# Kernel optimization log

Measured on AMD Instinct MI355X. Metric: run time of the kernel, lower is better.

The kernel has to match this reference:

```python
import jax, jax.numpy as jnp
import numpy as np

B, T, H = 8192, 24, 1024


def setup_inputs() -> dict:
    key = jax.random.key(0)
    ks = jax.random.split(key, 16)
    n = lambda k, shp, s=1.0: (jax.random.normal(k, shp, dtype=jnp.float32) * s)
    return {
        "x": n(ks[0], (B, T, 1)),
        "h1_0": n(ks[1], (B, H), 0.02),
        "c1_0": n(ks[2], (B, H), 0.02),
        "h2_0": n(ks[3], (B, H), 0.02),
        "c2_0": n(ks[4], (B, H), 0.02),
        "W_ih1": n(ks[5], (4 * H, 1), 0.05),
        "W_hh1": n(ks[6], (4 * H, H), 0.02),
        "b_ih1": n(ks[7], (4 * H,), 0.02),
        "b_hh1": n(ks[8], (4 * H,), 0.02),
        "W_ih2": n(ks[9], (4 * H, H), 0.02),
        "W_hh2": n(ks[10], (4 * H, H), 0.02),
        "b_ih2": n(ks[11], (4 * H,), 0.02),
        "b_hh2": n(ks[12], (4 * H,), 0.02),
        "W_out": n(ks[13], (2, H), 0.02),
        "b_out": jnp.array([0.2, -0.2], dtype=jnp.float32),
    }


def _lstm_cell(x_t, h, c, W_ih, W_hh, b_ih, b_hh):
    # PyTorch LSTMCell: gates ordered (i, f, g, o)
    gates = x_t @ W_ih.T + b_ih + h @ W_hh.T + b_hh  # [B, 4H]
    i, f, g, o = jnp.split(gates, 4, axis=-1)
    c_new = jax.nn.sigmoid(f) * c + jax.nn.sigmoid(i) * jnp.tanh(g)
    h_new = jax.nn.sigmoid(o) * jnp.tanh(c_new)
    return h_new, c_new


def reference(x, h1_0, c1_0, h2_0, c2_0,
              W_ih1, W_hh1, b_ih1, b_hh1,
              W_ih2, W_hh2, b_ih2, b_hh2,
              W_out, b_out):
    xs = jnp.transpose(x, (1, 0, 2))  # [T, B, 1]

    def step(carry, x_t):
        h1, c1, h2, c2 = carry
        h1, c1 = _lstm_cell(x_t, h1, c1, W_ih1, W_hh1, b_ih1, b_hh1)
        h2, c2 = _lstm_cell(h1, h2, c2, W_ih2, W_hh2, b_ih2, b_hh2)
        return (h1, c1, h2, c2), None

    (h1, c1, h2, c2), _ = jax.lax.scan(step, (h1_0, c1_0, h2_0, c2_0), xs)
    return h2 @ W_out.T + b_out  # [B, 2]
```

## Files before the change

kernel.cpp:

```cpp
#include <hip/hip_runtime.h>
#include <hip/hip_bf16.h>
#include <stdint.h>

#define B_SZ 8192
#define T_SZ 24
#define H_SZ 1024
#define G4   4096

typedef __attribute__((ext_vector_type(8))) short bf16x8;
typedef __attribute__((ext_vector_type(4))) float f32x4;

__device__ __forceinline__ int perm_old(int p) {
    int gate = (p >> 4) & 3;
    int unit = ((p >> 6) << 4) | (p & 15);
    return gate * 1024 + unit;
}

__global__ void k_prep_w1(const float* __restrict__ Whh1, __hip_bfloat16* __restrict__ dst) {
    int i = blockIdx.x * blockDim.x + threadIdx.x;
    int p = i >> 10, k = i & 1023;
    dst[i] = __float2bfloat16(Whh1[(size_t)perm_old(p) * 1024 + k]);
}

__global__ void k_prep_w2(const float* __restrict__ Wih2, const float* __restrict__ Whh2,
                          __hip_bfloat16* __restrict__ dst) {
    int i = blockIdx.x * blockDim.x + threadIdx.x;
    int p = i >> 11, k = i & 2047;
    int old = perm_old(p);
    float v = (k < 1024) ? Wih2[(size_t)old * 1024 + k] : Whh2[(size_t)old * 1024 + (k - 1024)];
    dst[i] = __float2bfloat16(v);
}

__global__ void k_prep_vec(const float* __restrict__ bih1, const float* __restrict__ bhh1,
                           const float* __restrict__ bih2, const float* __restrict__ bhh2,
                           const float* __restrict__ Wih1,
                           float* __restrict__ b1p, float* __restrict__ b2p,
                           float* __restrict__ w1p) {
    int p = blockIdx.x * blockDim.x + threadIdx.x;
    if (p >= G4) return;
    int old = perm_old(p);
    b1p[p] = bih1[old] + bhh1[old];
    b2p[p] = bih2[old] + bhh2[old];
    w1p[p] = Wih1[old];
}

__global__ void k_xT(const float* __restrict__ x, float* __restrict__ xT) {
    int i = blockIdx.x * blockDim.x + threadIdx.x;
    if (i >= B_SZ * T_SZ) return;
    int b = i / T_SZ, t = i % T_SZ;
    xT[t * B_SZ + b] = x[i];
}

__global__ void k_init_state(const float* __restrict__ h1_0, const float* __restrict__ c1_0,
                             const float* __restrict__ h2_0, const float* __restrict__ c2_0,
                             __hip_bfloat16* __restrict__ A2_0, __hip_bfloat16* __restrict__ A2_1,
                             float* __restrict__ c1, float* __restrict__ c2) {
    int i = blockIdx.x * blockDim.x + threadIdx.x;
    if (i >= B_SZ * H_SZ) return;
    int b = i >> 10, j = i & 1023;
    A2_1[(size_t)b * 2048 + j]        = __float2bfloat16(h1_0[i]);
    A2_0[(size_t)b * 2048 + 1024 + j] = __float2bfloat16(h2_0[i]);
    c1[i] = c1_0[i];
    c2[i] = c2_0[i];
}

#define BM 256
#define BN 256
#define BK 64

template<int LAYER>
__global__ __launch_bounds__(512, 2)
void k_gemm_cell(const __hip_bfloat16* __restrict__ A, int lda,
                 const __hip_bfloat16* __restrict__ Bw, int ldb, int K,
                 const float* __restrict__ biasp, const float* __restrict__ wih1p,
                 const float* __restrict__ xT, int t,
                 float* __restrict__ c, __hip_bfloat16* __restrict__ hout) {
    __shared__ short As[2][BM][BK];
    __shared__ short Bs[2][BN][BK];
    const int tid  = threadIdx.x;
    const int lane = tid & 63;
    const int wid  = tid >> 6;

    const int bid = blockIdx.x;
    const int xcd = bid & 7;
    const int i   = bid >> 3;
    const int ml  = (i & 7) | ((i >> 5) << 3);
    const int nl  = (i >> 3) & 3;
    const int m0  = ((xcd & 1) * 16 + ml) * BM;
    const int n0  = ((xcd >> 1) * 4 + nl) * BN;

    const int wm = wid >> 2;
    const int wn = wid & 3;
    const int fr = lane & 15;
    const int kg = lane >> 4;

    const __hip_bfloat16* Abase = A  + (size_t)m0 * lda;
    const __hip_bfloat16* Bbase = Bw + (size_t)n0 * ldb;

    f32x4 acc[8][4];
#pragma unroll
    for (int ii = 0; ii < 8; ++ii)
#pragma unroll
        for (int j = 0; j < 4; ++j) acc[ii][j] = (f32x4)0.f;

    auto stage8A = [&](int buf, int lr0, int kcol) {
        int lr = lr0 + (lane >> 3);
        int cr = lane & 7;
        int scol = ((cr ^ (lr & 7)) << 3);
        const __hip_bfloat16* gp = Abase + (size_t)lr * lda + kcol + scol;
        __builtin_amdgcn_global_load_lds(
            (const __attribute__((address_space(1))) void*)gp,
            (__attribute__((address_space(3))) void*)(&As[buf][lr0][0]), 16, 0, 0);
    };
    auto stage8B = [&](int buf, int lr0, int kcol) {
        int lr = lr0 + (lane >> 3);
        int cr = lane & 7;
        int scol = ((cr ^ (lr & 7)) << 3);
        const __hip_bfloat16* gp = Bbase + (size_t)lr * ldb + kcol + scol;
        __builtin_amdgcn_global_load_lds(
            (const __attribute__((address_space(1))) void*)gp,
            (__attribute__((address_space(3))) void*)(&Bs[buf][lr0][0]), 16, 0, 0);
    };
    auto stage_u1 = [&](int kt, int buf) {
#pragma unroll
        for (int j = 0; j < 2; ++j) {
            int rr0 = (wid * 2 + j) * 8;
            int lr0 = (rr0 < 64) ? rr0 : rr0 + 64;
            stage8A(buf, lr0, kt * BK);
        }
    };
    auto stage_u2 = [&](int kt, int buf) {
#pragma unroll
        for (int j = 0; j < 2; ++j) {
            int rr0 = (wid * 2 + j) * 8;
            int lr0 = (rr0 < 64) ? rr0 + 64 : rr0 + 128;
            stage8A(buf, lr0, kt * BK);
        }
    };
    auto stage_u3 = [&](int kt, int buf) {
#pragma unroll
        for (int j = 0; j < 2; ++j) {
            int rr0 = (wid * 2 + j) * 8;
            int lr0 = ((rr0 >> 5) << 6) + (rr0 & 31);
            stage8B(buf, lr0, kt * BK);
        }
    };
    auto stage_u4 = [&](int kt, int buf) {
#pragma unroll
        for (int j = 0; j < 2; ++j) {
            int rr0 = (wid * 2 + j) * 8;
            int lr0 = ((rr0 >> 5) << 6) + 32 + (rr0 & 31);
            stage8B(buf, lr0, kt * BK);
        }
    };

    auto rdA = [&](int buf, int m, int ks) -> bf16x8 {
        int row = wm * 128 + m * 16 + fr;
        int chunk = (ks * 4 + kg) ^ (row & 7);
        return *(const bf16x8*)&As[buf][row][chunk * 8];
    };
    auto rdB = [&](int buf, int n, int ks) -> bf16x8 {
        int row = wn * 64 + n * 16 + fr;
        int chunk = (ks * 4 + kg) ^ (row & 7);
        return *(const bf16x8*)&Bs[buf][row][chunk * 8];
    };

    const int NK = K >> 6;

    stage_u1(0, 0); stage_u3(0, 0); stage_u2(0, 0); stage_u4(0, 0);
    stage_u1(1, 1); stage_u3(1, 1);
    asm volatile("s_waitcnt vmcnt(8)" ::: "memory");
    __builtin_amdgcn_s_barrier();

    bf16x8 a0[4][2], a1[4][2], b0[2][2], b1[2][2];

    for (int kt = 0; kt < NK; ++kt) {
        const int buf = kt & 1;

#pragma unroll
        for (int m = 0; m < 4; ++m)
#pragma unroll
            for (int ks = 0; ks < 2; ++ks) a0[m][ks] = rdA(buf, m, ks);
#pragma unroll
        for (int n = 0; n < 2; ++n)
#pragma unroll
            for (int ks = 0; ks < 2; ++ks) b0[n][ks] = rdB(buf, n, ks);
        if (kt + 1 < NK) stage_u2(kt + 1, buf ^ 1);
        asm volatile("s_waitcnt lgkmcnt(8)" ::: "memory");
        __builtin_amdgcn_s_barrier();
        asm volatile("s_waitcnt lgkmcnt(0)" ::: "memory");
        __builtin_amdgcn_s_setprio(1);
#pragma unroll
        for (int ks = 0; ks < 2; ++ks)
#pragma unroll
            for (int m = 0; m < 4; ++m)
#pragma unroll
                for (int n = 0; n < 2; ++n)
                    acc[m][n] = __builtin_amdgcn_mfma_f32_16x16x32_bf16(a0[m][ks], b0[n][ks], acc[m][n], 0, 0, 0);
        __builtin_amdgcn_s_setprio(0);
        if (kt + 1 < NK) asm volatile("s_waitcnt vmcnt(6)" ::: "memory");
        else             asm volatile("s_waitcnt vmcnt(0)" ::: "memory");
        __builtin_amdgcn_s_barrier();

#pragma unroll
        for (int n = 0; n < 2; ++n)
#pragma unroll
            for (int ks = 0; ks < 2; ++ks) b1[n][ks] = rdB(buf, 2 + n, ks);
        if (kt + 1 < NK) stage_u4(kt + 1, buf ^ 1);
        __builtin_amdgcn_s_barrier();
        asm volatile("s_waitcnt lgkmcnt(0)" ::: "memory");
        __builtin_amdgcn_s_setprio(1);
#pragma unroll
        for (int ks = 0; ks < 2; ++ks)
#pragma unroll
            for (int m = 0; m < 4; ++m)
#pragma unroll
                for (int n = 0; n < 2; ++n)
                    acc[m][2 + n] = __builtin_amdgcn_mfma_f32_16x16x32_bf16(a0[m][ks], b1[n][ks], acc[m][2 + n], 0, 0, 0);
        __builtin_amdgcn_s_setprio(0);
        __builtin_amdgcn_s_barrier();

#pragma unroll
        for (int m = 0; m < 4; ++m)
#pragma unroll
            for (int ks = 0; ks < 2; ++ks) a1[m][ks] = rdA(buf, 4 + m, ks);
        if (kt + 2 < NK) stage_u1(kt + 2, buf);
        __builtin_amdgcn_s_barrier();
        asm volatile("s_waitcnt lgkmcnt(0)" ::: "memory");
        __builtin_amdgcn_s_setprio(1);
#pragma unroll
        for (int ks = 0; ks < 2; ++ks)
#pragma unroll
            for (int m = 0; m < 4; ++m)
#pragma unroll
                for (int n = 0; n < 2; ++n)
                    acc[4 + m][n] = __builtin_amdgcn_mfma_f32_16x16x32_bf16(a1[m][ks], b0[n][ks], acc[4 + m][n], 0, 0, 0);
        __builtin_amdgcn_s_setprio(0);
        __builtin_amdgcn_s_barrier();

        if (kt + 2 < NK) stage_u3(kt + 2, buf);
        __builtin_amdgcn_s_barrier();
        __builtin_amdgcn_s_setprio(1);
#pragma unroll
        for (int ks = 0; ks < 2; ++ks)
#pragma unroll
            for (int m = 0; m < 4; ++m)
#pragma unroll
                for (int n = 0; n < 2; ++n)
                    acc[4 + m][2 + n] = __builtin_amdgcn_mfma_f32_16x16x32_bf16(a1[m][ks], b1[n][ks], acc[4 + m][2 + n], 0, 0, 0);
        __builtin_amdgcn_s_setprio(0);
        if (kt + 2 < NK)      asm volatile("s_waitcnt vmcnt(6)" ::: "memory");
        else if (kt + 1 < NK) asm volatile("s_waitcnt vmcnt(4)" ::: "memory");
        __builtin_amdgcn_s_barrier();
    }

    float biasv[4], xwv[4];
#pragma unroll
    for (int n = 0; n < 4; ++n) {
        int col = n0 + wn * 64 + n * 16 + fr;
        biasv[n] = biasp[col];
        if (LAYER == 1) xwv[n] = wih1p[col];
    }
    const int u = ((n0 >> 6) + wn) * 16 + fr;

#pragma unroll
    for (int m = 0; m < 8; ++m) {
        int rbase = m0 + wm * 128 + m * 16 + (lane >> 4) * 4;
#pragma unroll
        for (int j = 0; j < 4; ++j) {
            int b = rbase + j;
            float gi = acc[m][0][j] + biasv[0];
            float gf = acc[m][1][j] + biasv[1];
            float gg = acc[m][2][j] + biasv[2];
            float go = acc[m][3][j] + biasv[3];
            if (LAYER == 1) {
                float xv = xT[t * B_SZ + b];
                gi += xv * xwv[0];
                gf += xv * xwv[1];
                gg += xv * xwv[2];
                go += xv * xwv[3];
            }
            float si = 1.f / (1.f + __expf(-gi));
            float sf = 1.f / (1.f + __expf(-gf));
            float so = 1.f / (1.f + __expf(-go));
            float tg = tanhf(gg);
            size_t ci = (size_t)b * H_SZ + u;
            float cn = sf * c[ci] + si * tg;
            c[ci] = cn;
            hout[(size_t)b * 2048 + u] = __float2bfloat16(so * tanhf(cn));
        }
    }
}

__global__ __launch_bounds__(256)
void k_out(const __hip_bfloat16* __restrict__ h2base, const float* __restrict__ Wout,
           const float* __restrict__ bout, float* __restrict__ out) {
    int gw   = (blockIdx.x * blockDim.x + threadIdx.x) >> 6;
    int lane = threadIdx.x & 63;
    if (gw >= B_SZ) return;
    const __hip_bfloat16* h = h2base + (size_t)gw * 2048;
    float a0 = 0.f, a1 = 0.f;
#pragma unroll
    for (int k = lane; k < 1024; k += 64) {
        float hv = __bfloat162float(h[k]);
        a0 += hv * Wout[k];
        a1 += hv * Wout[1024 + k];
    }
    for (int off = 32; off; off >>= 1) {
        a0 += __shfl_down(a0, off);
        a1 += __shfl_down(a1, off);
    }
    if (lane == 0) {
        out[gw * 2 + 0] = a0 + bout[0];
        out[gw * 2 + 1] = a1 + bout[1];
    }
}

extern "C" void kernel_launch(void* const* d_in, const int* in_sizes, int n_in,
                              void* d_out, int out_size, void* d_ws, size_t ws_size,
                              hipStream_t stream) {
    const float* x    = (const float*)d_in[0];
    const float* h1_0 = (const float*)d_in[1];
    const float* c1_0 = (const float*)d_in[2];
    const float* h2_0 = (const float*)d_in[3];
    const float* c2_0 = (const float*)d_in[4];
    const float* Wih1 = (const float*)d_in[5];
    const float* Whh1 = (const float*)d_in[6];
    const float* bih1 = (const float*)d_in[7];
    const float* bhh1 = (const float*)d_in[8];
    const float* Wih2 = (const float*)d_in[9];
    const float* Whh2 = (const float*)d_in[10];
    const float* bih2 = (const float*)d_in[11];
    const float* bhh2 = (const float*)d_in[12];
    const float* Wout = (const float*)d_in[13];
    const float* bout = (const float*)d_in[14];
    float* out = (float*)d_out;
    (void)in_sizes; (void)n_in; (void)out_size; (void)ws_size;

    uint8_t* ws = (uint8_t*)d_ws;
    size_t off = 0;
    auto alloc = [&](size_t bytes) { void* p = ws + off; off += (bytes + 255) & ~(size_t)255; return p; };
    __hip_bfloat16* A2_0  = (__hip_bfloat16*)alloc((size_t)B_SZ * 2048 * 2);
    __hip_bfloat16* A2_1  = (__hip_bfloat16*)alloc((size_t)B_SZ * 2048 * 2);
    float*          c1    = (float*)alloc((size_t)B_SZ * H_SZ * 4);
    float*          c2    = (float*)alloc((size_t)B_SZ * H_SZ * 4);
    __hip_bfloat16* Whh1p = (__hip_bfloat16*)alloc((size_t)G4 * H_SZ * 2);
    __hip_bfloat16* Wcat2p= (__hip_bfloat16*)alloc((size_t)G4 * 2048 * 2);
    float*          bias1p= (float*)alloc(G4 * 4);
    float*          bias2p= (float*)alloc(G4 * 4);
    float*          wih1p = (float*)alloc(G4 * 4);
    float*          xT    = (float*)alloc((size_t)T_SZ * B_SZ * 4);

    __hip_bfloat16* A2[2] = { A2_0, A2_1 };

    k_prep_w1<<<(G4 * H_SZ + 255) / 256, 256, 0, stream>>>(Whh1, Whh1p);
    k_prep_w2<<<(G4 * 2048 + 255) / 256, 256, 0, stream>>>(Wih2, Whh2, Wcat2p);
    k_prep_vec<<<(G4 + 255) / 256, 256, 0, stream>>>(bih1, bhh1, bih2, bhh2, Wih1,
                                                     bias1p, bias2p, wih1p);
    k_xT<<<(B_SZ * T_SZ + 255) / 256, 256, 0, stream>>>(x, xT);
    k_init_state<<<(B_SZ * H_SZ + 255) / 256, 256, 0, stream>>>(h1_0, c1_0, h2_0, c2_0,
                                                                A2_0, A2_1, c1, c2);

    const int gemm_blocks = (B_SZ / BM) * (G4 / BN);

    for (int t = 0; t < T_SZ; ++t) {
        __hip_bfloat16* Pprev = A2[(t + 1) & 1];
        __hip_bfloat16* Pt    = A2[t & 1];
        k_gemm_cell<1><<<gemm_blocks, 512, 0, stream>>>(
            (const __hip_bfloat16*)Pprev, 2048, Whh1p, 1024, 1024,
            bias1p, wih1p, xT, t, c1, Pt);
        k_gemm_cell<2><<<gemm_blocks, 512, 0, stream>>>(
            (const __hip_bfloat16*)Pt, 2048, Wcat2p, 2048, 2048,
            bias2p, nullptr, nullptr, 0, c2, A2[(t + 1) & 1] + 1024);
    }
    k_out<<<(B_SZ * 64 + 255) / 256, 256, 0, stream>>>(A2_0 + 1024, Wout, bout, out);
}
```

Measured before the change: 5.555 ms.

## Wavefront-fuse layer-1 step t+1 with layer-2 step t in one launch

```diff
diff --git a/kernel.cpp b/kernel.cpp
--- a/kernel.cpp
+++ b/kernel.cpp
@@ -14,6 +14,16 @@
     int gate = (p >> 4) & 3;
     int unit = ((p >> 6) << 4) | (p & 15);
     return gate * 1024 + unit;
+}
+
+__device__ __forceinline__ float fast_sigmoid(float x) {
+    return 1.f / (1.f + __expf(-x));
+}
+__device__ __forceinline__ float fast_tanh(float x) {
+    float ax = __builtin_fabsf(x);
+    float e  = __expf(2.f * ax);
+    float r  = 1.f - 2.f / (e + 1.f);
+    return __builtin_copysignf(r, x);
 }
 
 __global__ void k_prep_w1(const float* __restrict__ Whh1, __hip_bfloat16* __restrict__ dst) {
@@ -68,13 +78,14 @@
 #define BN 256
 #define BK 64
 
-template<int LAYER>
 __global__ __launch_bounds__(512, 2)
-void k_gemm_cell(const __hip_bfloat16* __restrict__ A, int lda,
-                 const __hip_bfloat16* __restrict__ Bw, int ldb, int K,
-                 const float* __restrict__ biasp, const float* __restrict__ wih1p,
-                 const float* __restrict__ xT, int t,
-                 float* __restrict__ c, __hip_bfloat16* __restrict__ hout) {
+void k_gemm_dual(const __hip_bfloat16* __restrict__ A,
+                 const __hip_bfloat16* __restrict__ W2, const float* __restrict__ bias2,
+                 float* __restrict__ c2p, __hip_bfloat16* __restrict__ hout2,
+                 const __hip_bfloat16* __restrict__ W1, const float* __restrict__ bias1,
+                 const float* __restrict__ wih1p, const float* __restrict__ xT, int t1,
+                 float* __restrict__ c1p, __hip_bfloat16* __restrict__ hout1,
+                 int mode) {
     __shared__ short As[2][BM][BK];
     __shared__ short Bs[2][BN][BK];
     const int tid  = threadIdx.x;
@@ -82,8 +93,22 @@
     const int wid  = tid >> 6;
 
     const int bid = blockIdx.x;
-    const int xcd = bid & 7;
-    const int i   = bid >> 3;
+    int role, sub;
+    if (mode == 1) { role = (bid >> 3) & 1; sub = ((bid >> 4) << 3) | (bid & 7); }
+    else           { role = (mode == 2) ? 1 : 0; sub = bid; }
+
+    const __hip_bfloat16* Bw;
+    const float* biasp;
+    const float* w1p;
+    float* c;
+    __hip_bfloat16* hout;
+    int ldb, K;
+    if (role == 0) { Bw = W2; ldb = 2048; K = 2048; biasp = bias2; w1p = nullptr; c = c2p; hout = hout2; }
+    else           { Bw = W1; ldb = 1024; K = 1024; biasp = bias1; w1p = wih1p;  c = c1p; hout = hout1; }
+    const int lda = 2048;
+
+    const int xcd = sub & 7;
+    const int i   = sub >> 3;
     const int ml  = (i & 7) | ((i >> 5) << 3);
     const int nl  = (i >> 3) & 3;
     const int m0  = ((xcd & 1) * 16 + ml) * BM;
@@ -105,8 +130,7 @@
 
     auto stage8A = [&](int buf, int lr0, int kcol) {
         int lr = lr0 + (lane >> 3);
-        int cr = lane & 7;
-        int scol = ((cr ^ (lr & 7)) << 3);
+        int scol = (((lane & 7) ^ (lr & 7)) << 3);
         const __hip_bfloat16* gp = Abase + (size_t)lr * lda + kcol + scol;
         __builtin_amdgcn_global_load_lds(
             (const __attribute__((address_space(1))) void*)gp,
@@ -114,8 +138,7 @@
     };
     auto stage8B = [&](int buf, int lr0, int kcol) {
         int lr = lr0 + (lane >> 3);
-        int cr = lane & 7;
-        int scol = ((cr ^ (lr & 7)) << 3);
+        int scol = (((lane & 7) ^ (lr & 7)) << 3);
         const __hip_bfloat16* gp = Bbase + (size_t)lr * ldb + kcol + scol;
         __builtin_amdgcn_global_load_lds(
             (const __attribute__((address_space(1))) void*)gp,
@@ -154,21 +177,19 @@
         }
     };
 
-    auto rdA = [&](int buf, int m, int ks) -> bf16x8 {
-        int row = wm * 128 + m * 16 + fr;
-        int chunk = (ks * 4 + kg) ^ (row & 7);
-        return *(const bf16x8*)&As[buf][row][chunk * 8];
-    };
-    auto rdB = [&](int buf, int n, int ks) -> bf16x8 {
-        int row = wn * 64 + n * 16 + fr;
-        int chunk = (ks * 4 + kg) ^ (row & 7);
-        return *(const bf16x8*)&Bs[buf][row][chunk * 8];
-    };
+    const int aoff = (wm * 128 + fr) * 64;
+    const int boff = (wn * 64 + fr) * 64;
+    const int ck8_0 = ((kg ^ (fr & 7)) << 3);
+    const int ck8_1 = (((4 + kg) ^ (fr & 7)) << 3);
+    const short* As0 = &As[0][0][0];
+    const short* As1 = &As[1][0][0];
+    const short* Bs0 = &Bs[0][0][0];
+    const short* Bs1 = &Bs[1][0][0];
 
     const int NK = K >> 6;
 
     stage_u1(0, 0); stage_u3(0, 0); stage_u2(0, 0); stage_u4(0, 0);
-    stage_u1(1, 1); stage_u3(1, 1);
+    stage_u1(1, 1); stage_u3(1, 1); stage_u4(1, 1); stage_u2(1, 1);
     asm volatile("s_waitcnt vmcnt(8)" ::: "memory");
     __builtin_amdgcn_s_barrier();
 
@@ -176,16 +197,19 @@
 
     for (int kt = 0; kt < NK; ++kt) {
         const int buf = kt & 1;
-
-#pragma unroll
-        for (int m = 0; m < 4; ++m)
-#pragma unroll
-            for (int ks = 0; ks < 2; ++ks) a0[m][ks] = rdA(buf, m, ks);
-#pragma unroll
-        for (int n = 0; n < 2; ++n)
-#pragma unroll
-            for (int ks = 0; ks < 2; ++ks) b0[n][ks] = rdB(buf, n, ks);
-        if (kt + 1 < NK) stage_u2(kt + 1, buf ^ 1);
+        const short* as = buf ? As1 : As0;
+        const short* bs = buf ? Bs1 : Bs0;
+
+#pragma unroll
+        for (int m = 0; m < 4; ++m) {
+            a0[m][0] = *(const bf16x8*)(as + aoff + m * 1024 + ck8_0);
+            a0[m][1] = *(const bf16x8*)(as + aoff + m * 1024 + ck8_1);
+        }
+#pragma unroll
+        for (int n = 0; n < 2; ++n) {
+            b0[n][0] = *(const bf16x8*)(bs + boff + n * 1024 + ck8_0);
+            b0[n][1] = *(const bf16x8*)(bs + boff + n * 1024 + ck8_1);
+        }
         asm volatile("s_waitcnt lgkmcnt(8)" ::: "memory");
         __builtin_amdgcn_s_barrier();
         asm volatile("s_waitcnt lgkmcnt(0)" ::: "memory");
@@ -198,15 +222,14 @@
                 for (int n = 0; n < 2; ++n)
                     acc[m][n] = __builtin_amdgcn_mfma_f32_16x16x32_bf16(a0[m][ks], b0[n][ks], acc[m][n], 0, 0, 0);
         __builtin_amdgcn_s_setprio(0);
-        if (kt + 1 < NK) asm volatile("s_waitcnt vmcnt(6)" ::: "memory");
-        else             asm volatile("s_waitcnt vmcnt(0)" ::: "memory");
-        __builtin_amdgcn_s_barrier();
-
-#pragma unroll
-        for (int n = 0; n < 2; ++n)
-#pragma unroll
-            for (int ks = 0; ks < 2; ++ks) b1[n][ks] = rdB(buf, 2 + n, ks);
-        if (kt + 1 < NK) stage_u4(kt + 1, buf ^ 1);
+        __builtin_amdgcn_s_barrier();
+
+#pragma unroll
+        for (int n = 0; n < 2; ++n) {
+            b1[n][0] = *(const bf16x8*)(bs + boff + (2 + n) * 1024 + ck8_0);
+            b1[n][1] = *(const bf16x8*)(bs + boff + (2 + n) * 1024 + ck8_1);
+        }
+        if (kt + 2 < NK) { stage_u1(kt + 2, buf); stage_u3(kt + 2, buf); }
         __builtin_amdgcn_s_barrier();
         asm volatile("s_waitcnt lgkmcnt(0)" ::: "memory");
         __builtin_amdgcn_s_setprio(1);
@@ -221,10 +244,11 @@
         __builtin_amdgcn_s_barrier();
 
 #pragma unroll
-        for (int m = 0; m < 4; ++m)
-#pragma unroll
-            for (int ks = 0; ks < 2; ++ks) a1[m][ks] = rdA(buf, 4 + m, ks);
-        if (kt + 2 < NK) stage_u1(kt + 2, buf);
+        for (int m = 0; m < 4; ++m) {
+            a1[m][0] = *(const bf16x8*)(as + aoff + (4 + m) * 1024 + ck8_0);
+            a1[m][1] = *(const bf16x8*)(as + aoff + (4 + m) * 1024 + ck8_1);
+        }
+        if (kt + 2 < NK) stage_u4(kt + 2, buf);
         __builtin_amdgcn_s_barrier();
         asm volatile("s_waitcnt lgkmcnt(0)" ::: "memory");
         __builtin_amdgcn_s_setprio(1);
@@ -238,7 +262,7 @@
         __builtin_amdgcn_s_setprio(0);
         __builtin_amdgcn_s_barrier();
 
-        if (kt + 2 < NK) stage_u3(kt + 2, buf);
+        if (kt + 2 < NK) stage_u2(kt + 2, buf);
         __builtin_amdgcn_s_barrier();
         __builtin_amdgcn_s_setprio(1);
 #pragma unroll
@@ -249,8 +273,8 @@
                 for (int n = 0; n < 2; ++n)
                     acc[4 + m][2 + n] = __builtin_amdgcn_mfma_f32_16x16x32_bf16(a1[m][ks], b1[n][ks], acc[4 + m][2 + n], 0, 0, 0);
         __builtin_amdgcn_s_setprio(0);
-        if (kt + 2 < NK)      asm volatile("s_waitcnt vmcnt(6)" ::: "memory");
-        else if (kt + 1 < NK) asm volatile("s_waitcnt vmcnt(4)" ::: "memory");
+        if (kt + 2 < NK)      asm volatile("s_waitcnt vmcnt(8)" ::: "memory");
+        else if (kt + 1 < NK) asm volatile("s_waitcnt vmcnt(0)" ::: "memory");
         __builtin_amdgcn_s_barrier();
     }
 
@@ -259,7 +283,7 @@
     for (int n = 0; n < 4; ++n) {
         int col = n0 + wn * 64 + n * 16 + fr;
         biasv[n] = biasp[col];
-        if (LAYER == 1) xwv[n] = wih1p[col];
+        xwv[n] = (w1p != nullptr) ? w1p[col] : 0.f;
     }
     const int u = ((n0 >> 6) + wn) * 16 + fr;
 
@@ -273,21 +297,21 @@
             float gf = acc[m][1][j] + biasv[1];
             float gg = acc[m][2][j] + biasv[2];
             float go = acc[m][3][j] + biasv[3];
-            if (LAYER == 1) {
-                float xv = xT[t * B_SZ + b];
+            if (w1p != nullptr) {
+                float xv = xT[t1 * B_SZ + b];
                 gi += xv * xwv[0];
                 gf += xv * xwv[1];
                 gg += xv * xwv[2];
                 go += xv * xwv[3];
             }
-            float si = 1.f / (1.f + __expf(-gi));
-            float sf = 1.f / (1.f + __expf(-gf));
-            float so = 1.f / (1.f + __expf(-go));
-            float tg = tanhf(gg);
+            float si = fast_sigmoid(gi);
+            float sf = fast_sigmoid(gf);
+            float so = fast_sigmoid(go);
+            float tg = fast_tanh(gg);
             size_t ci = (size_t)b * H_SZ + u;
             float cn = sf * c[ci] + si * tg;
             c[ci] = cn;
-            hout[(size_t)b * 2048 + u] = __float2bfloat16(so * tanhf(cn));
+            hout[(size_t)b * 2048 + u] = __float2bfloat16(so * fast_tanh(cn));
         }
     }
 }
@@ -361,17 +385,27 @@
     k_init_state<<<(B_SZ * H_SZ + 255) / 256, 256, 0, stream>>>(h1_0, c1_0, h2_0, c2_0,
                                                                 A2_0, A2_1, c1, c2);
 
-    const int gemm_blocks = (B_SZ / BM) * (G4 / BN);
-
-    for (int t = 0; t < T_SZ; ++t) {
-        __hip_bfloat16* Pprev = A2[(t + 1) & 1];
-        __hip_bfloat16* Pt    = A2[t & 1];
-        k_gemm_cell<1><<<gemm_blocks, 512, 0, stream>>>(
-            (const __hip_bfloat16*)Pprev, 2048, Whh1p, 1024, 1024,
-            bias1p, wih1p, xT, t, c1, Pt);
-        k_gemm_cell<2><<<gemm_blocks, 512, 0, stream>>>(
-            (const __hip_bfloat16*)Pt, 2048, Wcat2p, 2048, 2048,
-            bias2p, nullptr, nullptr, 0, c2, A2[(t + 1) & 1] + 1024);
-    }
+    k_gemm_dual<<<512, 512, 0, stream>>>(
+        (const __hip_bfloat16*)A2_1,
+        Wcat2p, bias2p, c2, A2_0 + 1024,
+        Whh1p, bias1p, wih1p, xT, 0, c1, A2_0,
+        2);
+
+    for (int t = 0; t < 23; ++t) {
+        __hip_bfloat16* Pt = A2[t & 1];
+        __hip_bfloat16* Pn = A2[(t + 1) & 1];
+        k_gemm_dual<<<1024, 512, 0, stream>>>(
+            (const __hip_bfloat16*)Pt,
+            Wcat2p, bias2p, c2, Pn + 1024,
+            Whh1p, bias1p, wih1p, xT, t + 1, c1, Pn,
+            1);
+    }
+
+    k_gemm_dual<<<512, 512, 0, stream>>>(
+        (const __hip_bfloat16*)A2_1,
+        Wcat2p, bias2p, c2, A2_0 + 1024,
+        Whh1p, bias1p, wih1p, xT, 0, c1, A2_0,
+        0);
+
     k_out<<<(B_SZ * 64 + 255) / 256, 256, 0, stream>>>(A2_0 + 1024, Wout, bout, out);
 }
```

Result: slower. 6.660 ms (+19.9%).
